# Performance work log

Hardware: AMD Instinct MI355X
Metric: run time of the kernel (lower is better)

The kernel has to match this reference:

```python
import jax, jax.numpy as jnp
import numpy as np

NX = 1024
N_HEAD = 16
HEAD_DIM = NX // N_HEAD
RPE_MAX = 20
LN_EPS = 1e-5


def _layernorm(h, g, b, eps=LN_EPS):
    mu = jnp.mean(h, axis=-1, keepdims=True)
    var = jnp.var(h, axis=-1, keepdims=True)
    return (h - mu) * jax.lax.rsqrt(var + eps) * g + b


def setup_inputs() -> dict:
    key = jax.random.key(0)
    ks = jax.random.split(key, 12)
    B, S = 2, 1024
    x = jax.random.normal(ks[0], (B, S, NX), dtype=jnp.float32)
    local_info = jax.random.normal(ks[1], (B, S, NX), dtype=jnp.float32)
    attention_mask = jnp.zeros((B, 1, 1, S), dtype=jnp.float32)
    pairwise_dist = jax.random.randint(ks[2], (B, S, S), -RPE_MAX, RPE_MAX + 1, dtype=jnp.int32)
    s = 0.02
    Wqkv = jax.random.normal(ks[3], (NX, 3 * NX), dtype=jnp.float32) * s
    bqkv = jnp.zeros((3 * NX,), dtype=jnp.float32)
    Wproj = jax.random.normal(ks[4], (NX, NX), dtype=jnp.float32) * s
    bproj = jnp.zeros((NX,), dtype=jnp.float32)
    rpek = jax.random.normal(ks[5], (2 * RPE_MAX + 1, HEAD_DIM), dtype=jnp.float32) * s
    ln1_g = jnp.ones((NX,), dtype=jnp.float32)
    ln1_b = jnp.zeros((NX,), dtype=jnp.float32)
    gate_W = jax.random.normal(ks[6], (2 * NX, NX), dtype=jnp.float32) * s
    return {"x": x, "local_info": local_info, "attention_mask": attention_mask,
            "pairwise_dist": pairwise_dist, "Wqkv": Wqkv, "bqkv": bqkv,
            "Wproj": Wproj, "bproj": bproj, "rpek": rpek,
            "ln1_g": ln1_g, "ln1_b": ln1_b, "gate_W": gate_W}


def reference(x, local_info, attention_mask, pairwise_dist, Wqkv, bqkv, Wproj, bproj, rpek, ln1_g, ln1_b, gate_W):
    B, S, _ = x.shape
    qkv = x @ Wqkv + bqkv                      # [B,S,3*NX]
    q, k, v = jnp.split(qkv, 3, axis=-1)
    q = q.reshape(B, S, N_HEAD, HEAD_DIM)
    k = k.reshape(B, S, N_HEAD, HEAD_DIM)
    v = v.reshape(B, S, N_HEAD, HEAD_DIM)
    # content scores [B,H,Q,K]
    w = jnp.einsum('bqhd,bkhd->bhqk', q, k)
    # relative-position bias: embedding lookup + per-query matmul
    k_rpe = rpek[pairwise_dist + RPE_MAX]      # [B,Q,K,D]
    w_rpe = jnp.einsum('bqhd,bqkd->bhqk', q, k_rpe)
    w = (w + w_rpe) / jnp.float32(HEAD_DIM) ** 0.5
    w = w + attention_mask
    p = jax.nn.softmax(w, axis=-1)
    a = jnp.einsum('bhqk,bkhd->bqhd', p, v).reshape(B, S, NX)
    a = a @ Wproj + bproj
    # residual + LN1
    h = _layernorm(x + a, ln1_g, ln1_b)
    # gated fusion of local and global info
    z = jax.nn.sigmoid(jnp.concatenate([local_info, h], axis=-1) @ gate_W)
    out = (1.0 - z) * h + z * local_info
    return out
```

## Files before the change

### kernel.cpp

```cpp
#include <hip/hip_runtime.h>
#include <hip/hip_bf16.h>

#define SEQ 1024
#define NH 16
#define HD 64
#define NXD 1024

typedef unsigned short u16;
typedef unsigned char u8;
typedef __attribute__((ext_vector_type(8))) short short8;
typedef __attribute__((ext_vector_type(4))) float f32x4;

__device__ __forceinline__ u16 f2bf(float f) {
    __hip_bfloat16 h = __float2bfloat16(f);
    u16 u; __builtin_memcpy(&u, &h, 2); return u;
}
__device__ __forceinline__ float bf2f(u16 u) {
    __hip_bfloat16 h; __builtin_memcpy(&h, &u, 2); return __bfloat162float(h);
}

__device__ __forceinline__ void gld16(const void* g, void* l) {
    __builtin_amdgcn_global_load_lds(
        (const __attribute__((address_space(1))) void*)g,
        (__attribute__((address_space(3))) void*)l, 16, 0, 0);
}

template<int N> __device__ __forceinline__ void waitcnt_vm() {
    asm volatile("s_waitcnt vmcnt(%0)" :: "n"(N) : "memory");
}
__device__ __forceinline__ void raw_barrier() {
    asm volatile("s_barrier" ::: "memory");
}

__device__ __forceinline__ int swz(int row, int k) { return k ^ ((row & 7) << 3); }

__device__ __forceinline__ void transpose_tile(const float* __restrict__ src,
        u16* __restrict__ dst, int R, int C, int bx, int by) {
    __shared__ float tile[32][33];
    int r0 = by * 32, c0 = bx * 32;
    int tr = threadIdx.x >> 3, tc = (threadIdx.x & 7) * 4;
    float4 v = *(const float4*)(src + (size_t)(r0 + tr) * C + c0 + tc);
    tile[tr][tc+0] = v.x; tile[tr][tc+1] = v.y; tile[tr][tc+2] = v.z; tile[tr][tc+3] = v.w;
    __syncthreads();
    int row = c0 + tr;
    int kk  = r0 + tc;
    u16* d = dst + (size_t)row * R + swz(row, kk);
    #pragma unroll
    for (int j = 0; j < 4; j++) d[j] = f2bf(tile[tc+j][tr]);
}

__global__ __launch_bounds__(256) void prep_all(const float* __restrict__ x,
        const float* __restrict__ local, const int* __restrict__ pd,
        const float* __restrict__ Wqkv, const float* __restrict__ Wproj,
        const float* __restrict__ gateW,
        u16* __restrict__ xb, u16* __restrict__ gateA, u8* __restrict__ pdu8,
        u16* __restrict__ WqkvT, u16* __restrict__ WprojT, u16* __restrict__ gateWT) {
    int bid = blockIdx.x;
    if (bid < 2048) {
        int i = (bid * 256 + threadIdx.x) * 4;
        int row = i >> 10, c = i & 1023;
        float4 v = *(const float4*)(x + i);
        u16* d = xb + (size_t)row * 1024 + swz(row, c);
        d[0] = f2bf(v.x); d[1] = f2bf(v.y); d[2] = f2bf(v.z); d[3] = f2bf(v.w);
    } else if (bid < 4096) {
        int i = ((bid - 2048) * 256 + threadIdx.x) * 4;
        int row = i >> 10, c = i & 1023;
        float4 v = *(const float4*)(local + i);
        u16* d = gateA + (size_t)row * 2048 + swz(row, c);
        d[0] = f2bf(v.x); d[1] = f2bf(v.y); d[2] = f2bf(v.z); d[3] = f2bf(v.w);
    } else if (bid < 6144) {
        int i = ((bid - 4096) * 256 + threadIdx.x) * 4;
        int4 v = *(const int4*)(pd + i);
        uchar4 o;
        o.x = (u8)(v.x + 20); o.y = (u8)(v.y + 20);
        o.z = (u8)(v.z + 20); o.w = (u8)(v.w + 20);
        *(uchar4*)(pdu8 + i) = o;
    } else if (bid < 9216) {
        int k = bid - 6144;  transpose_tile(Wqkv,  WqkvT,  1024, 3072, k % 96, k / 96);
    } else if (bid < 10240) {
        int k = bid - 9216;  transpose_tile(Wproj, WprojT, 1024, 1024, k % 32, k / 32);
    } else {
        int k = bid - 10240; transpose_tile(gateW, gateWT, 2048, 1024, k % 32, k / 32);
    }
}

template<int BM, int BN, int EPI, int CHX, int CHY>
__global__ __launch_bounds__(256) void gemm_bt(
        const u16* __restrict__ A, int lda, const u16* __restrict__ BT, int K,
        const float* __restrict__ bias, float* __restrict__ out_f,
        u16* __restrict__ oq, u16* __restrict__ ok, u16* __restrict__ ov,
        const u16* __restrict__ h16, const float* __restrict__ loc32,
        float* __restrict__ outg) {
    const int MT = BM / 32, NT = BN / 32;
    const int LPT = BM / 32 + BN / 32;
    __shared__ u16 Al[2][BM * 64];
    __shared__ u16 Bl[2][BN * 64];
    int t = threadIdx.x, lane = t & 63, wid = t >> 6;
    int quad = lane >> 4, l16 = lane & 15;
    int id = blockIdx.x + (CHX * 4) * blockIdx.y;
    int xcd = id & 7, li = id >> 3;
    int bxs = (xcd & 3) * CHX + li % CHX;
    int bys = (xcd >> 2) * CHY + li / CHX;
    int m0 = bys * BM, n0 = bxs * BN;
    int waveM = wid >> 1, waveN = wid & 1;
    f32x4 acc[MT][NT] = {};

    auto stage = [&](int buf, int k0) {
        #pragma unroll
        for (int i = 0; i < BM / 32; i++) {
            int c = t + i * 256;
            gld16(A + (size_t)(m0 + (c >> 3)) * lda + k0 + (c & 7) * 8,
                  &Al[buf][(c & ~63) * 8]);
        }
        #pragma unroll
        for (int i = 0; i < BN / 32; i++) {
            int c = t + i * 256;
            gld16(BT + (size_t)(n0 + (c >> 3)) * K + k0 + (c & 7) * 8,
                  &Bl[buf][(c & ~63) * 8]);
        }
    };

    const int NTILES = K >> 6;
    stage(0, 0);
    for (int tt = 0; tt < NTILES; tt++) {
        int cur = tt & 1;
        raw_barrier();
        if (tt + 1 < NTILES) {
            stage(cur ^ 1, (tt + 1) << 6);
            waitcnt_vm<LPT>();
        } else {
            waitcnt_vm<0>();
        }
        raw_barrier();
        const u16* Ac = Al[cur];
        const u16* Bc = Bl[cur];
        short8 af[MT][2], bfr[NT][2];
        #pragma unroll
        for (int s = 0; s < 2; s++) {
            int xk = (s * 4 + quad) ^ (l16 & 7);
            #pragma unroll
            for (int mt = 0; mt < MT; mt++)
                af[mt][s] = *(const short8*)&Ac[((waveM * (BM / 2) + mt * 16 + l16) * 8 + xk) * 8];
            #pragma unroll
            for (int nt = 0; nt < NT; nt++)
                bfr[nt][s] = *(const short8*)&Bc[((waveN * (BN / 2) + nt * 16 + l16) * 8 + xk) * 8];
        }
        #pragma unroll
        for (int mt = 0; mt < MT; mt++)
            #pragma unroll
            for (int nt = 0; nt < NT; nt++) {
                acc[mt][nt] = __builtin_amdgcn_mfma_f32_16x16x32_bf16(af[mt][0], bfr[nt][0], acc[mt][nt], 0, 0, 0);
                acc[mt][nt] = __builtin_amdgcn_mfma_f32_16x16x32_bf16(af[mt][1], bfr[nt][1], acc[mt][nt], 0, 0, 0);
            }
    }
    #pragma unroll
    for (int mt = 0; mt < MT; mt++)
        #pragma unroll
        for (int nt = 0; nt < NT; nt++)
            #pragma unroll
            for (int r = 0; r < 4; r++) {
                int row = m0 + waveM * (BM / 2) + mt * 16 + quad * 4 + r;
                int col = n0 + waveN * (BN / 2) + nt * 16 + l16;
                float val = acc[mt][nt][r];
                if (EPI == 0) {
                    val += bias[col];
                    int b = row >> 10, s = row & 1023;
                    int sec = col >> 10, cc = col & 1023;
                    int h = cc >> 6, d = cc & 63;
                    u16 bv = f2bf(val);
                    size_t bh = (size_t)(b * NH + h);
                    if (sec == 0)      oq[(bh * SEQ + s) * HD + d] = bv;
                    else if (sec == 1) ok[(bh * SEQ + s) * HD + swz(s, d)] = bv;
                    else               ov[((bh * 16 + (s >> 6)) * 64 + d) * 64 + swz(d, s & 63)] = bv;
                } else if (EPI == 1) {
                    out_f[(size_t)row * 1024 + col] = val + bias[col];
                } else {
                    float z = 1.f / (1.f + __expf(-val));
                    size_t idx = (size_t)row * 1024 + col;
                    float hv = bf2f(h16[(size_t)row * 2048 + 1024 + swz(row, col)]);
                    outg[idx] = (1.f - z) * hv + z * loc32[idx];
                }
            }
}

__global__ __launch_bounds__(256) void attn_kernel(
        const u16* __restrict__ qb, const u16* __restrict__ kmat,
        const u16* __restrict__ vTb, const float* __restrict__ rpek,
        const u8* __restrict__ pdu8, const float* __restrict__ mask,
        u16* __restrict__ aoutb) {
    __shared__ u16 Kl[64 * 64];
    __shared__ u16 Vl[64 * 64];
    __shared__ u16 Pl[4][8 * 16 * 8];
    __shared__ u16 qr_lds[64 * 48];
    __shared__ u8 pdl[64 * 80];
    int t = threadIdx.x, lane = t & 63, wid = t >> 6;
    int quad = lane >> 4, l16 = lane & 15;

    int id = blockIdx.x;
    int xcd = id & 7, j = id >> 3;
    int b = xcd >> 2;
    int head = ((xcd & 3) << 2) | (j >> 4);
    int qblk = (j & 15) << 6;
    int bh = (b << 4) | head;
    int q0 = qblk + wid * 16;

    short8 aq[2];
    #pragma unroll
    for (int s = 0; s < 2; s++)
        aq[s] = *(const short8*)(qb + ((size_t)bh * SEQ + q0 + l16) * HD + s * 32 + quad * 8);

    #pragma unroll
    for (int nt = 0; nt < 3; nt++) {
        int n = nt * 16 + l16;
        const float* rp = rpek + (size_t)(n < 41 ? n : 40) * HD;
        f32x4 acc = {0.f, 0.f, 0.f, 0.f};
        #pragma unroll
        for (int s = 0; s < 2; s++) {
            float4 f0 = *(const float4*)(rp + s * 32 + quad * 8);
            float4 f1 = *(const float4*)(rp + s * 32 + quad * 8 + 4);
            short8 bf;
            bf[0] = (short)f2bf(f0.x); bf[1] = (short)f2bf(f0.y);
            bf[2] = (short)f2bf(f0.z); bf[3] = (short)f2bf(f0.w);
            bf[4] = (short)f2bf(f1.x); bf[5] = (short)f2bf(f1.y);
            bf[6] = (short)f2bf(f1.z); bf[7] = (short)f2bf(f1.w);
            acc = __builtin_amdgcn_mfma_f32_16x16x32_bf16(aq[s], bf, acc, 0, 0, 0);
        }
        if (n < 41) {
            #pragma unroll
            for (int r = 0; r < 4; r++)
                qr_lds[(wid * 16 + quad * 4 + r) * 48 + n] = f2bf(acc[r]);
        }
    }

    f32x4 o[4] = {};
    float lrow[4] = {0.f, 0.f, 0.f, 0.f};
    u16* Pw = Pl[wid];
    const u8* pdbase = pdu8 + ((size_t)b * SEQ + qblk) * SEQ;
    for (int kt = 0; kt < 16; kt++) {
        int k0 = kt * 64;
        const u16* kbase = kmat + ((size_t)bh * SEQ + k0) * HD;
        const u16* vbase = vTb + (((size_t)bh * 16 + kt) * 64) * 64;
        __syncthreads();
        #pragma unroll
        for (int i = 0; i < 2; i++) {
            int c = t + i * 256;
            gld16(kbase + (size_t)c * 8, &Kl[(c & ~63) * 8]);
            gld16(vbase + (size_t)c * 8, &Vl[(c & ~63) * 8]);
        }
        {
            int qrow = t >> 2, kj = (t & 3) * 16;
            uint4 pv = *(const uint4*)(pdbase + (size_t)qrow * SEQ + k0 + kj);
            *(uint4*)&pdl[qrow * 80 + kj] = pv;
        }
        __syncthreads();
        #pragma unroll
        for (int ks = 0; ks < 4; ks++) {
            f32x4 a = {0.f, 0.f, 0.f, 0.f};
            #pragma unroll
            for (int dh = 0; dh < 2; dh++) {
                short8 bk = *(short8*)&Kl[((ks * 16 + l16) * 8 + ((dh * 4 + quad) ^ (l16 & 7))) * 8];
                a = __builtin_amdgcn_mfma_f32_16x16x32_bf16(aq[dh], bk, a, 0, 0, 0);
            }
            int kcol = k0 + ks * 16 + l16;
            float mk = mask[b * SEQ + kcol];
            int kcl = ks * 16 + l16;
            #pragma unroll
            for (int r = 0; r < 4; r++) {
                int ql = wid * 16 + quad * 4 + r;
                int pdv = pdl[ql * 80 + kcl];
                float rpe = bf2f(qr_lds[ql * 48 + pdv]);
                float sc = (a[r] + rpe) * 0.125f + mk;
                float p = __expf(fminf(sc, 30.f));
                lrow[r] += p;
                Pw[((kcl >> 3) * 16 + quad * 4 + r) * 8 + (kcl & 7)] = f2bf(p);
            }
        }
        asm volatile("s_waitcnt lgkmcnt(0)" ::: "memory");
        #pragma unroll
        for (int ks2 = 0; ks2 < 2; ks2++) {
            short8 pa = *(short8*)&Pw[((ks2 * 4 + quad) * 16 + l16) * 8];
            #pragma unroll
            for (int dt = 0; dt < 4; dt++) {
                short8 vv = *(short8*)&Vl[((dt * 16 + l16) * 8 + ((ks2 * 4 + quad) ^ (l16 & 7))) * 8];
                o[dt] = __builtin_amdgcn_mfma_f32_16x16x32_bf16(pa, vv, o[dt], 0, 0, 0);
            }
        }
    }
    #pragma unroll
    for (int r = 0; r < 4; r++) {
        #pragma unroll
        for (int off = 1; off < 16; off <<= 1)
            lrow[r] += __shfl_xor(lrow[r], off, 16);
    }
    #pragma unroll
    for (int r = 0; r < 4; r++) {
        int arow = b * SEQ + q0 + quad * 4 + r;
        float inv = 1.f / lrow[r];
        #pragma unroll
        for (int dt = 0; dt < 4; dt++) {
            int col = head * HD + dt * 16 + l16;
            aoutb[(size_t)arow * NXD + swz(arow, col)] = f2bf(o[dt][r] * inv);
        }
    }
}

__device__ __forceinline__ float block_sum(float v, float* sred) {
    #pragma unroll
    for (int o = 32; o > 0; o >>= 1) v += __shfl_down(v, o, 64);
    int lane = threadIdx.x & 63, wid = threadIdx.x >> 6;
    __syncthreads();
    if (lane == 0) sred[wid] = v;
    __syncthreads();
    return sred[0] + sred[1] + sred[2] + sred[3];
}

__global__ __launch_bounds__(256) void ln_kernel(const float* __restrict__ x,
        const float* __restrict__ a, const float* __restrict__ g,
        const float* __restrict__ bln, u16* __restrict__ gateA) {
    int row = blockIdx.x;
    __shared__ float sred[4];
    float vals[4];
    float s = 0.f;
    #pragma unroll
    for (int i = 0; i < 4; i++) {
        int c = threadIdx.x + i * 256;
        vals[i] = x[(size_t)row * NXD + c] + a[(size_t)row * NXD + c];
        s += vals[i];
    }
    s = block_sum(s, sred);
    float mu = s * (1.f / NXD);
    float vs = 0.f;
    #pragma unroll
    for (int i = 0; i < 4; i++) { float d = vals[i] - mu; vs += d * d; }
    vs = block_sum(vs, sred);
    float rstd = rsqrtf(vs * (1.f / NXD) + 1e-5f);
    #pragma unroll
    for (int i = 0; i < 4; i++) {
        int c = threadIdx.x + i * 256;
        float hv = (vals[i] - mu) * rstd * g[c] + bln[c];
        gateA[(size_t)row * 2048 + 1024 + swz(row, c)] = f2bf(hv);
    }
}

extern "C" void kernel_launch(void* const* d_in, const int* in_sizes, int n_in,
                              void* d_out, int out_size, void* d_ws, size_t ws_size,
                              hipStream_t stream) {
    const float* x     = (const float*)d_in[0];
    const float* local = (const float*)d_in[1];
    const float* mask  = (const float*)d_in[2];
    const int*   pd    = (const int*)d_in[3];
    const float* Wqkv  = (const float*)d_in[4];
    const float* bqkv  = (const float*)d_in[5];
    const float* Wproj = (const float*)d_in[6];
    const float* bproj = (const float*)d_in[7];
    const float* rpek  = (const float*)d_in[8];
    const float* ln_g  = (const float*)d_in[9];
    const float* ln_b  = (const float*)d_in[10];
    const float* gateW = (const float*)d_in[11];
    float* out = (float*)d_out;

    char* ws = (char*)d_ws;
    const size_t MB = 1u << 20;
    u16*   xb    = (u16*)(ws + 0);
    u16*   WqkvT = (u16*)(ws + 4 * MB);
    u16*   WprojT= (u16*)(ws + 10 * MB);
    u16*   qb    = (u16*)(ws + 12 * MB);
    u16*   kb    = (u16*)(ws + 16 * MB);
    float* pout  = (float*)(ws + 16 * MB);
    u16*   vTb   = (u16*)(ws + 24 * MB);
    u16*   gateA = (u16*)(ws + 34 * MB);
    u8*    pdu8  = (u8*)(ws + 42 * MB);
    u16*   gateWT= (u16*)(ws + 44 * MB);
    u16*   aoutb = xb;

    prep_all<<<12288, 256, 0, stream>>>(x, local, pd, Wqkv, Wproj, gateW,
            xb, gateA, pdu8, WqkvT, WprojT, gateWT);
    gemm_bt<128, 64, 0, 12, 8><<<dim3(48, 16), 256, 0, stream>>>(xb, 1024, WqkvT, 1024, bqkv,
            nullptr, qb, kb, vTb, nullptr, nullptr, nullptr);
    attn_kernel<<<512, 256, 0, stream>>>(qb, kb, vTb, rpek, pdu8, mask, aoutb);
    gemm_bt<64, 64, 1, 4, 16><<<dim3(16, 32), 256, 0, stream>>>(aoutb, 1024, WprojT, 1024, bproj,
            pout, nullptr, nullptr, nullptr, nullptr, nullptr, nullptr);
    ln_kernel<<<2048, 256, 0, stream>>>(x, pout, ln_g, ln_b, gateA);
    gemm_bt<64, 64, 2, 4, 16><<<dim3(16, 32), 256, 0, stream>>>(gateA, 2048, gateWT, 2048, nullptr,
            nullptr, nullptr, nullptr, nullptr, gateA, local, out);
}
```

Before: 223.8 us.

## Split attention over key halves and merge partials in a combine kernel

```diff
diff --git a/kernel.cpp b/kernel.cpp
--- a/kernel.cpp
+++ b/kernel.cpp
@@ -187,7 +187,7 @@
         const u16* __restrict__ qb, const u16* __restrict__ kmat,
         const u16* __restrict__ vTb, const float* __restrict__ rpek,
         const u8* __restrict__ pdu8, const float* __restrict__ mask,
-        u16* __restrict__ aoutb) {
+        u16* __restrict__ po0, u16* __restrict__ po1, float* __restrict__ pl) {
     __shared__ u16 Kl[64 * 64];
     __shared__ u16 Vl[64 * 64];
     __shared__ u16 Pl[4][8 * 16 * 8];
@@ -199,8 +199,9 @@
     int id = blockIdx.x;
     int xcd = id & 7, j = id >> 3;
     int b = xcd >> 2;
-    int head = ((xcd & 3) << 2) | (j >> 4);
-    int qblk = (j & 15) << 6;
+    int head = ((xcd & 3) << 2) | (j >> 5);
+    int qblk = ((j >> 1) & 15) << 6;
+    int sp = j & 1;
     int bh = (b << 4) | head;
     int q0 = qblk + wid * 16;
 
@@ -236,10 +237,10 @@
     float lrow[4] = {0.f, 0.f, 0.f, 0.f};
     u16* Pw = Pl[wid];
     const u8* pdbase = pdu8 + ((size_t)b * SEQ + qblk) * SEQ;
-    for (int kt = 0; kt < 16; kt++) {
-        int k0 = kt * 64;
+    for (int kt = 0; kt < 8; kt++) {
+        int k0 = sp * 512 + kt * 64;
         const u16* kbase = kmat + ((size_t)bh * SEQ + k0) * HD;
-        const u16* vbase = vTb + (((size_t)bh * 16 + kt) * 64) * 64;
+        const u16* vbase = vTb + (((size_t)bh * 16 + (k0 >> 6)) * 64) * 64;
         __syncthreads();
         #pragma unroll
         for (int i = 0; i < 2; i++) {
@@ -292,16 +293,32 @@
         for (int off = 1; off < 16; off <<= 1)
             lrow[r] += __shfl_xor(lrow[r], off, 16);
     }
+    u16* po = sp ? po1 : po0;
     #pragma unroll
     for (int r = 0; r < 4; r++) {
-        int arow = b * SEQ + q0 + quad * 4 + r;
-        float inv = 1.f / lrow[r];
-        #pragma unroll
-        for (int dt = 0; dt < 4; dt++) {
-            int col = head * HD + dt * 16 + l16;
-            aoutb[(size_t)arow * NXD + swz(arow, col)] = f2bf(o[dt][r] * inv);
-        }
-    }
+        int row = bh * SEQ + q0 + quad * 4 + r;
+        #pragma unroll
+        for (int dt = 0; dt < 4; dt++)
+            po[(size_t)row * 64 + dt * 16 + l16] = f2bf(o[dt][r]);
+        if (l16 == 0)
+            pl[sp * 32768 + row] = lrow[r];
+    }
+}
+
+__global__ __launch_bounds__(256) void attn_combine(const u16* __restrict__ po0,
+        const u16* __restrict__ po1, const float* __restrict__ pl,
+        u16* __restrict__ aoutb) {
+    int idx = blockIdx.x * 256 + threadIdx.x;
+    int row = idx >> 6, d = idx & 63;
+    float l0 = pl[row], l1 = pl[32768 + row];
+    float inv = 1.f / (l0 + l1);
+    float o0 = bf2f(po0[(size_t)row * 64 + d]);
+    float o1 = bf2f(po1[(size_t)row * 64 + d]);
+    float val = (o0 + o1) * inv;
+    int bh = row >> 10, qrow = row & 1023;
+    int b = bh >> 4, h = bh & 15;
+    int arow = b * SEQ + qrow;
+    aoutb[(size_t)arow * NXD + swz(arow, h * HD + d)] = f2bf(val);
 }
 
 __device__ __forceinline__ float block_sum(float v, float* sred) {
@@ -363,9 +380,12 @@
     const size_t MB = 1u << 20;
     u16*   xb    = (u16*)(ws + 0);
     u16*   WqkvT = (u16*)(ws + 4 * MB);
+    u16*   po0   = (u16*)(ws + 4 * MB);
+    float* pl    = (float*)(ws + 8 * MB);
     u16*   WprojT= (u16*)(ws + 10 * MB);
     u16*   qb    = (u16*)(ws + 12 * MB);
     u16*   kb    = (u16*)(ws + 16 * MB);
+    u16*   po1   = (u16*)(ws + 20 * MB);
     float* pout  = (float*)(ws + 16 * MB);
     u16*   vTb   = (u16*)(ws + 24 * MB);
     u16*   gateA = (u16*)(ws + 34 * MB);
@@ -377,7 +397,9 @@
             xb, gateA, pdu8, WqkvT, WprojT, gateWT);
     gemm_bt<128, 64, 0, 12, 8><<<dim3(48, 16), 256, 0, stream>>>(xb, 1024, WqkvT, 1024, bqkv,
             nullptr, qb, kb, vTb, nullptr, nullptr, nullptr);
-    attn_kernel<<<512, 256, 0, stream>>>(qb, kb, vTb, rpek, pdu8, mask, aoutb);
+    attn_kernel<<<1024, 256, 0, stream>>>(qb, kb, vTb, rpek, pdu8, mask,
+            po0, po1, pl);
+    attn_combine<<<8192, 256, 0, stream>>>(po0, po1, pl, aoutb);
     gemm_bt<64, 64, 1, 4, 16><<<dim3(16, 32), 256, 0, stream>>>(aoutb, 1024, WprojT, 1024, bproj,
             pout, nullptr, nullptr, nullptr, nullptr, nullptr, nullptr);
     ln_kernel<<<2048, 256, 0, stream>>>(x, pout, ln_g, ln_b, gateA);
```

Measured after the change: 213.7 us. -4.5%, faster.
